# Kernel tuning notes

Measured on AMD Instinct MI355X. Metric: run time of the kernel, lower is better.

Reference implementation:

```python
import math
import jax, jax.numpy as jnp
import numpy as np

HEAD_DIM = 128
NUM_HEADS = 16
ROPE_BASE = 10000.0


def _rope_tables(seq_len, dim, dtype):
    inv_freq = 1.0 / (ROPE_BASE ** (jnp.arange(0, dim, 2, dtype=jnp.float32) / dim))
    t = jnp.arange(seq_len, dtype=jnp.float32)
    freqs = jnp.einsum('i,j->ij', t, inv_freq)          # [S, D/2]
    emb = jnp.concatenate([freqs, freqs], axis=-1)       # [S, D]
    return jnp.cos(emb).astype(dtype), jnp.sin(emb).astype(dtype)


def _rotate_half(x):
    x1, x2 = jnp.split(x, 2, axis=-1)
    return jnp.concatenate([-x2, x1], axis=-1)


def _apply_rope(x, cos, sin):
    # x: [B, S, H, D]; cos/sin: [S, D] broadcast over batch and heads
    return x * cos[None, :, None, :] + _rotate_half(x) * sin[None, :, None, :]


def setup_inputs() -> dict:
    key = jax.random.key(0)
    k1, k2, k3 = jax.random.split(key, 3)
    B, S, dim = 2, 2048, 2048
    out_dim = (NUM_HEADS + 2 * NUM_HEADS) * HEAD_DIM  # kvph=1 -> 3*H*D = 6144
    x = jax.random.normal(k1, (B, S, dim), dtype=jnp.float32)
    w_qkv = jax.random.normal(k2, (out_dim, dim), dtype=jnp.float32) * 0.02
    w_out = jax.random.normal(k3, (dim, NUM_HEADS * HEAD_DIM), dtype=jnp.float32) * 0.02
    return {"x": x, "w_qkv": w_qkv, "w_out": w_out}


def reference(x, w_qkv, w_out):
    B, S, _ = x.shape
    H, D = NUM_HEADS, HEAD_DIM
    qkv = jnp.einsum('bsd,od->bso', x, w_qkv)            # [B, S, 3*H*D]
    qkv = qkv.reshape(B, S, 3 * H, D)
    q = qkv[:, :, :H, :]                                 # [B, S, H, D]
    k = qkv[:, :, H:2 * H, :]
    v = qkv[:, :, 2 * H:, :]
    cos, sin = _rope_tables(S, D, x.dtype)
    q = _apply_rope(q, cos, sin)
    k = _apply_rope(k, cos, sin)
    scale = 1.0 / math.sqrt(D)
    logits = jnp.einsum('bqhd,bkhd->bhqk', q, k) * scale  # [B, H, S, S]
    attn = jax.nn.softmax(logits.astype(jnp.float32), axis=-1).astype(logits.dtype)
    out = jnp.einsum('bhqk,bkhd->bqhd', attn, v)          # [B, S, H, D]
    out = out.reshape(B, S, H * D)
    return jnp.einsum('bso,do->bsd', out, w_out)
```

## Files before the change

kernel.cpp:

```cpp
#include <hip/hip_runtime.h>
#include <math.h>
#include <stdint.h>

typedef unsigned short u16;
typedef unsigned int u32;
typedef float f32x4 __attribute__((ext_vector_type(4)));
typedef __bf16 bf16x8 __attribute__((ext_vector_type(8)));

typedef const __attribute__((address_space(1))) u32* gas1;
typedef __attribute__((address_space(3))) u32* las3;

#define B_ 2
#define S_ 2048
#define DM_ 2048
#define H_ 16
#define HD_ 128
#define NO_ 6144
#define M_ 4096

__device__ __forceinline__ u16 f2bf(float f) {
  u32 u = __float_as_uint(f);
  u32 r = (u + 0x7fffu + ((u >> 16) & 1u)) >> 16;
  return (u16)r;
}
__device__ __forceinline__ float bf2f(u16 h) {
  return __uint_as_float(((u32)h) << 16);
}

__global__ void cvt_bf16(const float* __restrict__ in, u16* __restrict__ out, int n) {
  int i = (blockIdx.x * blockDim.x + threadIdx.x) * 4;
  int stride = gridDim.x * blockDim.x * 4;
  for (; i < n; i += stride) {
    float4 v = *(const float4*)(in + i);
    ushort4 o;
    o.x = f2bf(v.x); o.y = f2bf(v.y); o.z = f2bf(v.z); o.w = f2bf(v.w);
    *(ushort4*)(out + i) = o;
  }
}

__global__ void rope_tables(float* __restrict__ ct, float* __restrict__ st) {
  int i = blockIdx.x * blockDim.x + threadIdx.x;
  int s = i >> 6, j = i & 63;
  float inv = powf(10000.0f, -(float)j / 64.0f);
  float f = (float)s * inv;
  ct[i] = cosf(f);
  st[i] = sinf(f);
}

__global__ __launch_bounds__(512, 2) void gemm8_bt(const u16* __restrict__ A,
                                                   const u16* __restrict__ B,
                                                   u16* __restrict__ C,
                                                   int M, int N, int K) {
  __shared__ u16 lds8[2][2][2][8192];
  const int t = threadIdx.x;
  const int w = t >> 6, l = t & 63, lr = l & 15, lg = l >> 4;
  const int wm = w >> 2, wn = w & 3;
  const int m0 = blockIdx.y * 256, n0 = blockIdx.x * 256;
  const int r0 = t >> 2;
  const int c = (t & 3) ^ ((t >> 3) & 3);
  const int swr = (lr >> 1) & 3;
  const u16* pA0 = A + (size_t)(m0 + r0) * K + c * 8;
  const u16* pB0 = B + (size_t)(n0 + r0) * K + c * 8;
  const size_t j1 = (size_t)128 * K;

  f32x4 acc[8][4] = {};
  bf16x8 af[8], bq[4];

  const int NT = K / 64, NI = NT / 2;

#define STG(T_, kh_, op_, buf_)                                                      \
  do {                                                                               \
    const u16* s_ = (op_ ? pB0 : pA0) + (T_) * 64 + (kh_) * 32;                      \
    u16* d_ = &lds8[buf_][op_][kh_][0] + w * 512;                                    \
    __builtin_amdgcn_global_load_lds((gas1)s_, (las3)d_, 16, 0, 0);                  \
    __builtin_amdgcn_global_load_lds((gas1)(s_ + j1), (las3)(d_ + 4096), 16, 0, 0);  \
  } while (0)

#define LDF(buf_, kh_)                                                            \
  do {                                                                            \
    const u16* a_ = &lds8[buf_][0][kh_][0];                                       \
    const u16* b_ = &lds8[buf_][1][kh_][0];                                       \
    _Pragma("unroll") for (int mi = 0; mi < 8; ++mi)                              \
        af[mi] = *(const bf16x8*)&a_[(wm * 128 + mi * 16 + lr) * 32 +             \
                                     ((lg ^ swr) * 8)];                           \
    _Pragma("unroll") for (int ni = 0; ni < 4; ++ni)                              \
        bq[ni] = *(const bf16x8*)&b_[(wn * 64 + ni * 16 + lr) * 32 +              \
                                     ((lg ^ swr) * 8)];                           \
  } while (0)

#define MFH(h_)                                                                \
  do {                                                                         \
    __builtin_amdgcn_s_setprio(1);                                             \
    _Pragma("unroll") for (int mi = 0; mi < 4; ++mi)                           \
        _Pragma("unroll") for (int ni = 0; ni < 4; ++ni)                       \
            acc[(h_) * 4 + mi][ni] = __builtin_amdgcn_mfma_f32_16x16x32_bf16(  \
                af[(h_) * 4 + mi], bq[ni], acc[(h_) * 4 + mi][ni], 0, 0, 0);   \
    __builtin_amdgcn_s_setprio(0);                                             \
  } while (0)

#define BAR() __builtin_amdgcn_s_barrier()
#define LGKM0() asm volatile("s_waitcnt lgkmcnt(0)" ::: "memory")
#define VM6() asm volatile("s_waitcnt vmcnt(6)" ::: "memory")

  STG(0, 0, 0, 0); STG(0, 0, 1, 0); STG(0, 1, 0, 0); STG(0, 1, 1, 0);
  STG(1, 0, 0, 1); STG(1, 0, 1, 1); STG(1, 1, 0, 1);
  VM6();
  BAR();

  for (int i = 0; i < NI; ++i) {
    const int T = 2 * i;
    const int Tp2 = (T + 2 < NT) ? T + 2 : NT - 1;
    const int Tp3 = (T + 3 < NT) ? T + 3 : NT - 1;
    LDF(0, 0);
    STG(T + 1, 1, 1, 1);
    BAR(); LGKM0(); MFH(0); BAR();
    STG(Tp2, 0, 0, 0);
    BAR(); MFH(1); BAR();
    LDF(0, 1);
    STG(Tp2, 0, 1, 0);
    BAR(); LGKM0(); MFH(0); BAR();
    STG(Tp2, 1, 0, 0);
    VM6(); BAR(); MFH(1); BAR();
    LDF(1, 0);
    STG(Tp2, 1, 1, 0);
    BAR(); LGKM0(); MFH(0); BAR();
    STG(Tp3, 0, 0, 1);
    BAR(); MFH(1); BAR();
    LDF(1, 1);
    STG(Tp3, 0, 1, 1);
    BAR(); LGKM0(); MFH(0); BAR();
    STG(Tp3, 1, 0, 1);
    VM6(); BAR(); MFH(1); BAR();
  }
  asm volatile("s_waitcnt vmcnt(0)" ::: "memory");
  BAR();

#pragma unroll
  for (int mi = 0; mi < 8; ++mi)
#pragma unroll
    for (int ni = 0; ni < 4; ++ni) {
      int row = m0 + wm * 128 + mi * 16 + lg * 4;
      int col = n0 + wn * 64 + ni * 16 + lr;
#pragma unroll
      for (int j = 0; j < 4; ++j)
        C[(size_t)(row + j) * N + col] = f2bf(acc[mi][ni][j]);
    }
#undef STG
#undef LDF
#undef MFH
#undef BAR
#undef LGKM0
#undef VM6
}

template <int OUT_BF16>
__global__ __launch_bounds__(256) void gemm_bt(const u16* __restrict__ A,
                                               const u16* __restrict__ B,
                                               void* __restrict__ Cv,
                                               int M, int N, int K) {
  __shared__ u16 lA[128 * 32];
  __shared__ u16 lB[128 * 32];
  const int t = threadIdx.x;
  const int m0 = blockIdx.y * 128, n0 = blockIdx.x * 128;
  const int w = t >> 6, l = t & 63, lr = l & 15, lg = l >> 4;
  const int wm = (w >> 1) * 64, wn = (w & 1) * 64;
  f32x4 acc[4][4] = {};
  const int srow = t >> 2;
  const int scol = ((t & 3) ^ ((t >> 3) & 3)) * 8;
  const int swr = (lr >> 1) & 3;
  const u16* Ag = A + (size_t)(m0 + srow) * K + scol;
  const u16* Bg = B + (size_t)(n0 + srow) * K + scol;

  for (int k0 = 0; k0 < K; k0 += 32) {
    __syncthreads();
#pragma unroll
    for (int i = 0; i < 2; i++) {
      __builtin_amdgcn_global_load_lds((gas1)(Ag + (size_t)i * 64 * K + k0),
                                       (las3)(lA + (i * 256 + w * 64) * 8), 16, 0, 0);
      __builtin_amdgcn_global_load_lds((gas1)(Bg + (size_t)i * 64 * K + k0),
                                       (las3)(lB + (i * 256 + w * 64) * 8), 16, 0, 0);
    }
    __syncthreads();
    bf16x8 af[4], bfr[4];
#pragma unroll
    for (int mi = 0; mi < 4; mi++)
      af[mi] = *(const bf16x8*)&lA[(wm + mi * 16 + lr) * 32 + (lg ^ swr) * 8];
#pragma unroll
    for (int ni = 0; ni < 4; ni++)
      bfr[ni] = *(const bf16x8*)&lB[(wn + ni * 16 + lr) * 32 + (lg ^ swr) * 8];
#pragma unroll
    for (int mi = 0; mi < 4; mi++)
#pragma unroll
      for (int ni = 0; ni < 4; ni++)
        acc[mi][ni] =
            __builtin_amdgcn_mfma_f32_16x16x32_bf16(af[mi], bfr[ni], acc[mi][ni], 0, 0, 0);
  }

#pragma unroll
  for (int mi = 0; mi < 4; mi++)
#pragma unroll
    for (int ni = 0; ni < 4; ni++) {
      int row = m0 + wm + mi * 16 + lg * 4;
      int col = n0 + wn + ni * 16 + lr;
      if (OUT_BF16) {
        u16* C = (u16*)Cv;
#pragma unroll
        for (int j = 0; j < 4; j++) C[(size_t)(row + j) * N + col] = f2bf(acc[mi][ni][j]);
      } else {
        float* C = (float*)Cv;
#pragma unroll
        for (int j = 0; j < 4; j++) C[(size_t)(row + j) * N + col] = acc[mi][ni][j];
      }
    }
}

__global__ void rope_apply(u16* __restrict__ qkv, const float* __restrict__ ct,
                           const float* __restrict__ st) {
  int i = blockIdx.x * blockDim.x + threadIdx.x;
  int j = i & 63;
  int hh = (i >> 6) & 31;
  int row = i >> 11;
  int s = row & (S_ - 1);
  int col = (hh < 16) ? hh * 128 : 2048 + (hh - 16) * 128;
  u16* p = qkv + (size_t)row * NO_ + col + j;
  float e1 = bf2f(p[0]), e2 = bf2f(p[64]);
  float c = ct[(s << 6) + j], sn = st[(s << 6) + j];
  float o1 = e1 * c - e2 * sn;
  float o2 = e2 * c + e1 * sn;
  if (hh < 16) {
    const float kq = 0.08838834764831845f * 1.4426950408889634f;
    o1 *= kq;
    o2 *= kq;
  }
  p[0] = f2bf(o1);
  p[64] = f2bf(o2);
}

__global__ __launch_bounds__(256) void transpose_v(const u16* __restrict__ qkv,
                                                   u16* __restrict__ vt) {
  __shared__ u16 lds[128 * 64];
  const int bh = blockIdx.y;
  const int b = bh >> 4, h = bh & 15;
  const int s0 = blockIdx.x * 64;
  const int t = threadIdx.x;
  union { uint4 v; u16 e[8]; } uu;
#pragma unroll
  for (int i = 0; i < 4; i++) {
    int s = i * 16 + (t >> 4);
    int dc = (t & 15) * 8;
    uu.v = *(const uint4*)(qkv + (size_t)(b * S_ + s0 + s) * NO_ + 4096 + h * 128 + dc);
#pragma unroll
    for (int q = 0; q < 8; q++) {
      int d = dc + q;
      lds[d * 64 + (s ^ (((d >> 3) & 7) << 3))] = uu.e[q];
    }
  }
  __syncthreads();
#pragma unroll
  for (int i = 0; i < 4; i++) {
    int d = i * 32 + (t >> 3);
    int sc = (t & 7) * 8;
    uint4 v = *(const uint4*)&lds[d * 64 + (sc ^ (((d >> 3) & 7) << 3))];
    *(uint4*)(vt + (size_t)(bh * 128 + d) * S_ + s0 + sc) = v;
  }
}

__global__ __launch_bounds__(256, 2) void flash_attn(const u16* __restrict__ qkv,
                                                     const u16* __restrict__ vt,
                                                     u16* __restrict__ ao) {
  __shared__ u16 lK[2][64 * 128];
  __shared__ u16 lV[2][128 * 64];
  __shared__ u16 lP[4][2][16 * 64];
  const int t = threadIdx.x;
  const int w = t >> 6, l = t & 63, lr = l & 15, lg = l >> 4;
  const int bh = blockIdx.y, b = bh >> 4, h = bh & 15;
  const int q0 = blockIdx.x * 128;

  bf16x8 qf[2][4];
#pragma unroll
  for (int g = 0; g < 2; g++) {
    const u16* Qg = qkv + (size_t)(b * S_ + q0 + w * 32 + g * 16 + lr) * NO_ + h * 128;
#pragma unroll
    for (int c = 0; c < 4; c++) qf[g][c] = *(const bf16x8*)(Qg + c * 32 + lg * 8);
  }

  f32x4 acc[2][8] = {};
  float m_run[2] = {-INFINITY, -INFINITY};
  float l_run[2] = {0.f, 0.f};

  const u16* ksrc[4];
  const u16* vsrc[4];
#pragma unroll
  for (int q = 0; q < 4; q++) {
    int rt = w * 16 + q * 4 + (l >> 4);
    int ck = (l & 15) ^ (rt & 15);
    ksrc[q] = qkv + (size_t)(b * S_ + rt) * NO_ + 2048 + h * 128 + ck * 8;
    int d = w * 32 + q * 8 + (l >> 3);
    int cv = (l & 7) ^ (d & 7);
    vsrc[q] = vt + (size_t)(bh * 128 + d) * S_ + cv * 8;
  }

#pragma unroll
  for (int q = 0; q < 4; q++) {
    __builtin_amdgcn_global_load_lds((gas1)ksrc[q],
                                     (las3)(lK[0] + (w * 16 + q * 4) * 128), 16, 0, 0);
    __builtin_amdgcn_global_load_lds((gas1)vsrc[q],
                                     (las3)(lV[0] + (w * 32 + q * 8) * 64), 16, 0, 0);
    ksrc[q] += (size_t)64 * NO_;
    vsrc[q] += 64;
  }
  __syncthreads();

  const int NT = S_ / 64;
  for (int kt = 0; kt < NT; kt++) {
    const int cur = kt & 1;
    if (kt + 1 < NT) {
#pragma unroll
      for (int q = 0; q < 4; q++) {
        __builtin_amdgcn_global_load_lds((gas1)ksrc[q],
                                         (las3)(lK[cur ^ 1] + (w * 16 + q * 4) * 128), 16, 0, 0);
        __builtin_amdgcn_global_load_lds((gas1)vsrc[q],
                                         (las3)(lV[cur ^ 1] + (w * 32 + q * 8) * 64), 16, 0, 0);
        ksrc[q] += (size_t)64 * NO_;
        vsrc[q] += 64;
      }
    }

    f32x4 sc[2][4];
#pragma unroll
    for (int g = 0; g < 2; g++)
#pragma unroll
      for (int cb = 0; cb < 4; cb++) sc[g][cb] = (f32x4){0.f, 0.f, 0.f, 0.f};
    __builtin_amdgcn_s_setprio(1);
#pragma unroll
    for (int cb = 0; cb < 4; cb++) {
      int r = cb * 16 + lr;
#pragma unroll
      for (int c = 0; c < 4; c++) {
        bf16x8 kf = *(const bf16x8*)&lK[cur][r * 128 + ((c * 32 + lg * 8) ^ ((r & 15) << 3))];
        sc[0][cb] = __builtin_amdgcn_mfma_f32_16x16x32_bf16(kf, qf[0][c], sc[0][cb], 0, 0, 0);
        sc[1][cb] = __builtin_amdgcn_mfma_f32_16x16x32_bf16(kf, qf[1][c], sc[1][cb], 0, 0, 0);
      }
    }
    __builtin_amdgcn_s_setprio(0);

    float tmax[2];
#pragma unroll
    for (int g = 0; g < 2; g++) {
      float v = sc[g][0][0];
#pragma unroll
      for (int cb = 0; cb < 4; cb++)
#pragma unroll
        for (int j = 0; j < 4; j++) v = fmaxf(v, sc[g][cb][j]);
      v = fmaxf(v, __shfl_xor(v, 16));
      v = fmaxf(v, __shfl_xor(v, 32));
      tmax[g] = v;
    }
    bool ok = (tmax[0] <= m_run[0] + 10.0f) && (tmax[1] <= m_run[1] + 10.0f);
    if (!__all(ok)) {
      float resc[2];
#pragma unroll
      for (int g = 0; g < 2; g++) {
        float mn = fmaxf(m_run[g], tmax[g]);
        resc[g] = exp2f(m_run[g] - mn);
        m_run[g] = mn;
        l_run[g] *= resc[g];
      }
#pragma unroll
      for (int g = 0; g < 2; g++)
#pragma unroll
        for (int j = 0; j < 4; j++) {
          float rj = __shfl(resc[g], lg * 4 + j);
#pragma unroll
          for (int nb = 0; nb < 8; nb++) acc[g][nb][j] *= rj;
        }
    }
#pragma unroll
    for (int g = 0; g < 2; g++) {
      float ps = 0.f;
#pragma unroll
      for (int cb = 0; cb < 4; cb++)
#pragma unroll
        for (int j = 0; j < 4; j++) {
          float p = exp2f(sc[g][cb][j] - m_run[g]);
          sc[g][cb][j] = p;
          ps += p;
        }
      ps += __shfl_xor(ps, 16);
      ps += __shfl_xor(ps, 32);
      l_run[g] += ps;
    }

#pragma unroll
    for (int g = 0; g < 2; g++) {
      u16* lPw = lP[w][g];
#pragma unroll
      for (int cb = 0; cb < 4; cb++) {
        ushort4 pk;
        pk.x = f2bf(sc[g][cb][0]);
        pk.y = f2bf(sc[g][cb][1]);
        pk.z = f2bf(sc[g][cb][2]);
        pk.w = f2bf(sc[g][cb][3]);
        *(ushort4*)&lPw[lr * 64 + ((cb * 16 + lg * 4) ^ ((lr & 7) << 3))] = pk;
      }
    }

    __builtin_amdgcn_s_setprio(1);
#pragma unroll
    for (int c2 = 0; c2 < 2; c2++) {
      bf16x8 pf0 = *(const bf16x8*)&lP[w][0][lr * 64 + ((c2 * 32 + lg * 8) ^ ((lr & 7) << 3))];
      bf16x8 pf1 = *(const bf16x8*)&lP[w][1][lr * 64 + ((c2 * 32 + lg * 8) ^ ((lr & 7) << 3))];
#pragma unroll
      for (int nb = 0; nb < 8; nb++) {
        int r = nb * 16 + lr;
        bf16x8 vf = *(const bf16x8*)&lV[cur][r * 64 + ((c2 * 32 + lg * 8) ^ ((r & 7) << 3))];
        acc[0][nb] = __builtin_amdgcn_mfma_f32_16x16x32_bf16(pf0, vf, acc[0][nb], 0, 0, 0);
        acc[1][nb] = __builtin_amdgcn_mfma_f32_16x16x32_bf16(pf1, vf, acc[1][nb], 0, 0, 0);
      }
    }
    __builtin_amdgcn_s_setprio(0);

    __syncthreads();
  }

#pragma unroll
  for (int g = 0; g < 2; g++) {
    float linv[4];
#pragma unroll
    for (int j = 0; j < 4; j++) linv[j] = 1.0f / __shfl(l_run[g], lg * 4 + j);
#pragma unroll
    for (int nb = 0; nb < 8; nb++)
#pragma unroll
      for (int j = 0; j < 4; j++) {
        int qrow = q0 + w * 32 + g * 16 + lg * 4 + j;
        ao[(size_t)(b * S_ + qrow) * 2048 + h * 128 + nb * 16 + lr] =
            f2bf(acc[g][nb][j] * linv[j]);
      }
  }
}

extern "C" void kernel_launch(void* const* d_in, const int* in_sizes, int n_in,
                              void* d_out, int out_size, void* d_ws, size_t ws_size,
                              hipStream_t stream) {
  const float* x = (const float*)d_in[0];
  const float* wqkv = (const float*)d_in[1];
  const float* wout = (const float*)d_in[2];
  float* out = (float*)d_out;

  char* ws = (char*)d_ws;
  u16* xbf = (u16*)(ws);
  u16* wqkvb = (u16*)(ws + ((size_t)16 << 20));
  u16* woutb = (u16*)(ws + ((size_t)40 << 20));
  u16* qkv = (u16*)(ws + ((size_t)48 << 20));
  u16* vtb = (u16*)(ws + ((size_t)96 << 20));
  float* ct = (float*)(ws + ((size_t)112 << 20));
  float* st = (float*)(ws + ((size_t)112 << 20) + ((size_t)1 << 19));
  u16* aout = xbf;

  cvt_bf16<<<4096, 256, 0, stream>>>(x, xbf, M_ * DM_);
  cvt_bf16<<<4096, 256, 0, stream>>>(wqkv, wqkvb, NO_ * DM_);
  cvt_bf16<<<4096, 256, 0, stream>>>(wout, woutb, DM_ * DM_);
  rope_tables<<<(S_ * 64) / 256, 256, 0, stream>>>(ct, st);
  gemm8_bt<<<dim3(NO_ / 256, M_ / 256), 512, 0, stream>>>(xbf, wqkvb, qkv, M_, NO_, DM_);
  rope_apply<<<(M_ * 32 * 64) / 256, 256, 0, stream>>>(qkv, ct, st);
  transpose_v<<<dim3(S_ / 64, B_ * H_), 256, 0, stream>>>(qkv, vtb);
  flash_attn<<<dim3(S_ / 128, B_ * H_), 256, 0, stream>>>(qkv, vtb, aout);
  gemm_bt<0><<<dim3(DM_ / 128, M_ / 128), 256, 0, stream>>>(aout, woutb, out, M_, DM_, DM_);
}
```

Baseline: 332.9 us.

## Shrink QKV GEMM tile to 128x256, add block swizzle, use packed bf16 convert

The QKV projection GEMM moves from 256x256 to 128x256 output tiles per block, doubling the grid to 768 blocks so the CUs are better covered. Block indices are remapped with an XCD-style swizzle to improve L2 locality, and the A/B LDS staging and vmcnt waits are rebalanced for the smaller A tile. In flash attention, softmax probabilities are converted to bf16 with the hardware v_cvt_pk_bf16_f32 instruction instead of software rounding. The smaller tile lowers arithmetic intensity per block and increases total global traffic.

```diff
diff --git a/kernel.cpp b/kernel.cpp
--- a/kernel.cpp
+++ b/kernel.cpp
@@ -51,11 +51,17 @@
                                                    const u16* __restrict__ B,
                                                    u16* __restrict__ C,
                                                    int M, int N, int K) {
-  __shared__ u16 lds8[2][2][2][8192];
+  __shared__ u16 lA8[2][2][128 * 32];
+  __shared__ u16 lB8[2][2][256 * 32];
   const int t = threadIdx.x;
   const int w = t >> 6, l = t & 63, lr = l & 15, lg = l >> 4;
   const int wm = w >> 2, wn = w & 3;
-  const int m0 = blockIdx.y * 256, n0 = blockIdx.x * 256;
+  const int nx = gridDim.x;
+  const int orig = blockIdx.y * nx + blockIdx.x;
+  const int cpx = (nx * gridDim.y) >> 3;
+  const int swz = (orig & 7) * cpx + (orig >> 3);
+  const int n0 = (swz % nx) * 256;
+  const int m0 = (swz / nx) * 128;
   const int r0 = t >> 2;
   const int c = (t & 3) ^ ((t >> 3) & 3);
   const int swr = (lr >> 1) & 3;
@@ -63,25 +69,32 @@
   const u16* pB0 = B + (size_t)(n0 + r0) * K + c * 8;
   const size_t j1 = (size_t)128 * K;
 
-  f32x4 acc[8][4] = {};
-  bf16x8 af[8], bq[4];
+  f32x4 acc[4][4] = {};
+  bf16x8 af[4], bq[4];
 
   const int NT = K / 64, NI = NT / 2;
 
-#define STG(T_, kh_, op_, buf_)                                                      \
+#define STGA(T_, kh_, buf_)                                                    \
+  do {                                                                         \
+    const u16* s_ = pA0 + (T_) * 64 + (kh_) * 32;                              \
+    u16* d_ = &lA8[buf_][kh_][0] + w * 512;                                    \
+    __builtin_amdgcn_global_load_lds((gas1)s_, (las3)d_, 16, 0, 0);            \
+  } while (0)
+
+#define STGB(T_, kh_, buf_)                                                          \
   do {                                                                               \
-    const u16* s_ = (op_ ? pB0 : pA0) + (T_) * 64 + (kh_) * 32;                      \
-    u16* d_ = &lds8[buf_][op_][kh_][0] + w * 512;                                    \
+    const u16* s_ = pB0 + (T_) * 64 + (kh_) * 32;                                    \
+    u16* d_ = &lB8[buf_][kh_][0] + w * 512;                                          \
     __builtin_amdgcn_global_load_lds((gas1)s_, (las3)d_, 16, 0, 0);                  \
     __builtin_amdgcn_global_load_lds((gas1)(s_ + j1), (las3)(d_ + 4096), 16, 0, 0);  \
   } while (0)
 
 #define LDF(buf_, kh_)                                                            \
   do {                                                                            \
-    const u16* a_ = &lds8[buf_][0][kh_][0];                                       \
-    const u16* b_ = &lds8[buf_][1][kh_][0];                                       \
-    _Pragma("unroll") for (int mi = 0; mi < 8; ++mi)                              \
-        af[mi] = *(const bf16x8*)&a_[(wm * 128 + mi * 16 + lr) * 32 +             \
+    const u16* a_ = &lA8[buf_][kh_][0];                                           \
+    const u16* b_ = &lB8[buf_][kh_][0];                                           \
+    _Pragma("unroll") for (int mi = 0; mi < 4; ++mi)                              \
+        af[mi] = *(const bf16x8*)&a_[(wm * 64 + mi * 16 + lr) * 32 +              \
                                      ((lg ^ swr) * 8)];                           \
     _Pragma("unroll") for (int ni = 0; ni < 4; ++ni)                              \
         bq[ni] = *(const bf16x8*)&b_[(wn * 64 + ni * 16 + lr) * 32 +              \
@@ -92,19 +105,19 @@
   do {                                                                         \
     __builtin_amdgcn_s_setprio(1);                                             \
     _Pragma("unroll") for (int mi = 0; mi < 4; ++mi)                           \
-        _Pragma("unroll") for (int ni = 0; ni < 4; ++ni)                       \
-            acc[(h_) * 4 + mi][ni] = __builtin_amdgcn_mfma_f32_16x16x32_bf16(  \
-                af[(h_) * 4 + mi], bq[ni], acc[(h_) * 4 + mi][ni], 0, 0, 0);   \
+        _Pragma("unroll") for (int nj = 0; nj < 2; ++nj)                       \
+            acc[mi][(h_) * 2 + nj] = __builtin_amdgcn_mfma_f32_16x16x32_bf16(  \
+                af[mi], bq[(h_) * 2 + nj], acc[mi][(h_) * 2 + nj], 0, 0, 0);   \
     __builtin_amdgcn_s_setprio(0);                                             \
   } while (0)
 
 #define BAR() __builtin_amdgcn_s_barrier()
 #define LGKM0() asm volatile("s_waitcnt lgkmcnt(0)" ::: "memory")
-#define VM6() asm volatile("s_waitcnt vmcnt(6)" ::: "memory")
-
-  STG(0, 0, 0, 0); STG(0, 0, 1, 0); STG(0, 1, 0, 0); STG(0, 1, 1, 0);
-  STG(1, 0, 0, 1); STG(1, 0, 1, 1); STG(1, 1, 0, 1);
-  VM6();
+#define VM4() asm volatile("s_waitcnt vmcnt(4)" ::: "memory")
+
+  STGA(0, 0, 0); STGB(0, 0, 0); STGA(0, 1, 0); STGB(0, 1, 0);
+  STGA(1, 0, 1); STGB(1, 0, 1); STGA(1, 1, 1);
+  VM4();
   BAR();
 
   for (int i = 0; i < NI; ++i) {
@@ -112,45 +125,46 @@
     const int Tp2 = (T + 2 < NT) ? T + 2 : NT - 1;
     const int Tp3 = (T + 3 < NT) ? T + 3 : NT - 1;
     LDF(0, 0);
-    STG(T + 1, 1, 1, 1);
+    STGB(T + 1, 1, 1);
     BAR(); LGKM0(); MFH(0); BAR();
-    STG(Tp2, 0, 0, 0);
+    STGA(Tp2, 0, 0);
     BAR(); MFH(1); BAR();
     LDF(0, 1);
-    STG(Tp2, 0, 1, 0);
+    STGB(Tp2, 0, 0);
     BAR(); LGKM0(); MFH(0); BAR();
-    STG(Tp2, 1, 0, 0);
-    VM6(); BAR(); MFH(1); BAR();
+    STGA(Tp2, 1, 0);
+    VM4(); BAR(); MFH(1); BAR();
     LDF(1, 0);
-    STG(Tp2, 1, 1, 0);
+    STGB(Tp2, 1, 0);
     BAR(); LGKM0(); MFH(0); BAR();
-    STG(Tp3, 0, 0, 1);
+    STGA(Tp3, 0, 1);
     BAR(); MFH(1); BAR();
     LDF(1, 1);
-    STG(Tp3, 0, 1, 1);
+    STGB(Tp3, 0, 1);
     BAR(); LGKM0(); MFH(0); BAR();
-    STG(Tp3, 1, 0, 1);
-    VM6(); BAR(); MFH(1); BAR();
+    STGA(Tp3, 1, 1);
+    VM4(); BAR(); MFH(1); BAR();
   }
   asm volatile("s_waitcnt vmcnt(0)" ::: "memory");
   BAR();
 
 #pragma unroll
-  for (int mi = 0; mi < 8; ++mi)
+  for (int mi = 0; mi < 4; ++mi)
 #pragma unroll
     for (int ni = 0; ni < 4; ++ni) {
-      int row = m0 + wm * 128 + mi * 16 + lg * 4;
+      int row = m0 + wm * 64 + mi * 16 + lg * 4;
       int col = n0 + wn * 64 + ni * 16 + lr;
 #pragma unroll
       for (int j = 0; j < 4; ++j)
         C[(size_t)(row + j) * N + col] = f2bf(acc[mi][ni][j]);
     }
-#undef STG
+#undef STGA
+#undef STGB
 #undef LDF
 #undef MFH
 #undef BAR
 #undef LGKM0
-#undef VM6
+#undef VM4
 }
 
 template <int OUT_BF16>
@@ -396,12 +410,13 @@
       u16* lPw = lP[w][g];
 #pragma unroll
       for (int cb = 0; cb < 4; cb++) {
-        ushort4 pk;
-        pk.x = f2bf(sc[g][cb][0]);
-        pk.y = f2bf(sc[g][cb][1]);
-        pk.z = f2bf(sc[g][cb][2]);
-        pk.w = f2bf(sc[g][cb][3]);
-        *(ushort4*)&lPw[lr * 64 + ((cb * 16 + lg * 4) ^ ((lr & 7) << 3))] = pk;
+        u32 p01, p23;
+        asm("v_cvt_pk_bf16_f32 %0, %1, %2" : "=v"(p01) : "v"(sc[g][cb][0]), "v"(sc[g][cb][1]));
+        asm("v_cvt_pk_bf16_f32 %0, %1, %2" : "=v"(p23) : "v"(sc[g][cb][2]), "v"(sc[g][cb][3]));
+        uint2 pk;
+        pk.x = p01;
+        pk.y = p23;
+        *(uint2*)&lPw[lr * 64 + ((cb * 16 + lg * 4) ^ ((lr & 7) << 3))] = pk;
       }
     }
 
@@ -461,7 +476,7 @@
   cvt_bf16<<<4096, 256, 0, stream>>>(wqkv, wqkvb, NO_ * DM_);
   cvt_bf16<<<4096, 256, 0, stream>>>(wout, woutb, DM_ * DM_);
   rope_tables<<<(S_ * 64) / 256, 256, 0, stream>>>(ct, st);
-  gemm8_bt<<<dim3(NO_ / 256, M_ / 256), 512, 0, stream>>>(xbf, wqkvb, qkv, M_, NO_, DM_);
+  gemm8_bt<<<dim3(NO_ / 256, M_ / 128), 512, 0, stream>>>(xbf, wqkvb, qkv, M_, NO_, DM_);
   rope_apply<<<(M_ * 32 * 64) / 256, 256, 0, stream>>>(qkv, ct, st);
   transpose_v<<<dim3(S_ / 64, B_ * H_), 256, 0, stream>>>(qkv, vtb);
   flash_attn<<<dim3(S_ / 128, B_ * H_), 256, 0, stream>>>(qkv, vtb, aout);
```

After: 346.7 us. 1.04x slower.
